# Performance work log

Hardware: AMD Instinct MI355X
Metric: run time of the kernel (lower is better)

Reference implementation:

```python
import jax, jax.numpy as jnp
import numpy as np

K = 7
PAD = K // 2
C = 24          # latent_dim
ITERS = 4


def conv2d(x, w, b):
    # x: (B, Cin, H, W), w: (Cout, Cin, kh, kw) -> (B, Cout, H, W), SAME padding
    y = jax.lax.conv_general_dilated(
        x, w, window_strides=(1, 1), padding='SAME',
        dimension_numbers=('NCHW', 'OIHW', 'NCHW'))
    return y + b[None, :, None, None]


def unfold(x, H, W):
    # F.unfold(x, K, padding=PAD).view(B, C, K*K, H, W)
    # ordering: for each channel, kernel offsets row-major (kh outer, kw inner)
    xp = jnp.pad(x, ((0, 0), (0, 0), (PAD, PAD), (PAD, PAD)))
    patches = jnp.stack(
        [xp[:, :, i:i + H, j:j + W] for i in range(K) for j in range(K)],
        axis=2)  # (B, C, K*K, H, W)
    return patches


def setup_inputs() -> dict:
    key = jax.random.key(0)
    ks = jax.random.split(key, 8)
    B, H, W = 2, 256, 256
    depth = jax.random.normal(ks[0], (B, 1, H, W), dtype=jnp.float32)
    texture = jax.random.normal(ks[1], (B, 3, H, W), dtype=jnp.float32)
    # depth_proj: Conv2d(1, C, 3, padding=1)
    w_dp = jax.random.normal(ks[2], (C, 1, 3, 3), dtype=jnp.float32) * 0.1
    b_dp = jax.random.normal(ks[3], (C,), dtype=jnp.float32) * 0.1
    # kernel_predictor: Conv2d(3, C*K*K, 3, padding=1) followed by softmax(dim=1)
    w_kp = jax.random.normal(ks[4], (C * K * K, 3, 3, 3), dtype=jnp.float32) * 0.1
    b_kp = jax.random.normal(ks[5], (C * K * K,), dtype=jnp.float32) * 0.1
    # to_depth: Conv2d(C, 1, 1)
    w_td = jax.random.normal(ks[6], (1, C, 1, 1), dtype=jnp.float32) * 0.1
    b_td = jax.random.normal(ks[7], (1,), dtype=jnp.float32) * 0.1
    return {'depth': depth, 'texture': texture,
            'w_dp': w_dp, 'b_dp': b_dp,
            'w_kp': w_kp, 'b_kp': b_kp,
            'w_td': w_td, 'b_td': b_td}


def reference(depth, texture, w_dp, b_dp, w_kp, b_kp, w_td, b_td):
    B, _, H, W = depth.shape
    depth_latent = conv2d(depth, w_dp, b_dp)                    # (B, C, H, W)
    logits = conv2d(texture, w_kp, b_kp)                        # (B, C*K*K, H, W)
    kernels = jax.nn.softmax(logits, axis=1)                    # softmax over full channel dim
    kernels = kernels.reshape(B, C, K * K, H, W)
    unfolded = unfold(depth_latent, H, W)                       # (B, C, K*K, H, W)
    for it in range(ITERS):
        diffused = jnp.sum(kernels * unfolded, axis=2)          # (B, C, H, W)
        if it < ITERS - 1:
            unfolded = unfold(diffused, H, W)
    fused_depth = conv2d(diffused, w_td, b_td)                  # (B, 1, H, W)
    return fused_depth
```

## Files before the change

kernel.cpp:

```cpp
#include <hip/hip_runtime.h>

#define BB   2
#define HH   256
#define WW   256
#define HWSZ (HH * WW)
#define CC   24
#define KSZ  7
#define KK   49
#define PADK 3
#define G    8
#define CPG  3
#define LSTR 24
#define CSTR (22 * LSTR)
#define LOG2E 1.44269504088896340736f

typedef __attribute__((ext_vector_type(8))) short short8;
typedef __attribute__((ext_vector_type(4))) float float4v;

__device__ __forceinline__ short f2bf(float x) {
  unsigned u = __builtin_bit_cast(unsigned, x);
  unsigned r = u + 0x7FFFu + ((u >> 16) & 1u);
  return (short)(r >> 16);
}
__device__ __forceinline__ float bf2f(short h) {
  unsigned u = ((unsigned)(unsigned short)h) << 16;
  return __builtin_bit_cast(float, u);
}

__global__ __launch_bounds__(256) void k_setup(
    const float* __restrict__ w_kp, const float* __restrict__ b_kp,
    const float* __restrict__ tex, short* __restrict__ wsW,
    short* __restrict__ wsB) {
  __shared__ float lt[3 * 324];
  __shared__ int lltk[32];
  int blk = blockIdx.x;
  if (blk < 192) {
    int s = blk & 1, mt = (blk >> 1) & 3, cg = blk >> 3;
    for (int idx = threadIdx.x; idx < 512; idx += 256) {
      int row = idx >> 5, k = idx & 31;
      int kk = mt * 16 + row;
      float v = 0.f;
      if (kk < KK && k < 28)
        v = ((k < 27) ? w_kp[((size_t)cg * KK + kk) * 27 + k]
                      : b_kp[cg * KK + kk]) * LOG2E;
      short hi = f2bf(v);
      short h = (s == 0) ? hi : f2bf(v - bf2f(hi));
      wsW[(size_t)blk * 512 + idx] = h;
    }
    return;
  }
  int tb = blk - 192;
  int b = tb >> 8, tile = tb & 255;
  int y0 = (tile >> 4) * 16, x0 = (tile & 15) * 16;
  int tid = threadIdx.x, lane = tid & 63, wv = tid >> 6;
  int q = lane >> 4, col = lane & 15;

  if (tid < 32) {
    int k = tid, v;
    if (k < 27) v = (k / 9) * 324 + ((k % 9) / 3) * 18 + (k % 3);
    else if (k == 27) v = -1;
    else v = -2;
    lltk[k] = v;
  }
  for (int idx = tid; idx < 972; idx += 256) {
    int ci = idx / 324, r = idx % 324;
    int iy = r / 18, ix = r % 18;
    int yy = y0 + iy - 1, xx = x0 + ix - 1;
    bool ok = (yy >= 0 && yy < HH && xx >= 0 && xx < WW);
    lt[idx] = ok ? tex[((size_t)b * 3 + ci) * HWSZ + yy * WW + xx] : 0.f;
  }
  __syncthreads();

  int tko[8];
#pragma unroll
  for (int j = 0; j < 8; ++j) tko[j] = lltk[q * 8 + j];
  int4* w4 = (int4*)wsB;
#pragma unroll
  for (int nt = 0; nt < 4; ++nt) {
    short8 hi, lo;
#pragma unroll
    for (int j = 0; j < 8; ++j) {
      int o = tko[j];
      float v = (o == -1) ? 1.f
                          : ((o == -2) ? 0.f : lt[o + (wv * 4 + nt) * 18 + col]);
      short h = f2bf(v);
      hi[j] = h;
      lo[j] = f2bf(v - bf2f(h));
    }
    size_t base = ((((size_t)(b * 256 + tile) * 4 + wv) * 4 + nt) * 2);
    w4[(base + 0) * 64 + lane] = __builtin_bit_cast(int4, hi);
    w4[(base + 1) * 64 + lane] = __builtin_bit_cast(int4, lo);
  }
}

template <bool FIRST, bool FINAL>
__global__ __launch_bounds__(256, 4) void k_diffuse_m(
    const float* __restrict__ depth, const float* __restrict__ src,
    const float* __restrict__ invZ, const float* __restrict__ w_dp,
    const float* __restrict__ b_dp, const short* __restrict__ wsW,
    const short* __restrict__ wsB, float* __restrict__ dst,
    float* __restrict__ part, const float* __restrict__ w_td,
    float* __restrict__ outp) {
  __shared__ __align__(16) short lw[24 * 512];
  __shared__ float lsrc[CPG * CSTR];
  __shared__ float ldp[FIRST ? 576 : 4];
  __shared__ int loffs[64];

  int b = blockIdx.z / G, g = blockIdx.z % G, c0 = g * CPG;
  int x0 = blockIdx.x * 16, y0 = blockIdx.y * 16;
  int tile = blockIdx.y * 16 + blockIdx.x;
  int tid = threadIdx.x, lane = tid & 63, wv = tid >> 6;
  int q = lane >> 4, col = lane & 15;

  if (tid < 64)
    loffs[tid] = (tid < KK) ? ((tid / 7) - 3) * LSTR + ((tid % 7) - 3) : 0;
  {
    const int4* s4 = (const int4*)(wsW + (size_t)g * 12288);
    int4* d4 = (int4*)lw;
#pragma unroll
    for (int i = 0; i < 6; ++i) d4[tid + i * 256] = s4[tid + i * 256];
  }
  if (FIRST) {
    for (int idx = tid; idx < 576; idx += 256) {
      int iy = idx / 24, ix = idx % 24;
      int yy = y0 + iy - 4, xx = x0 + ix - 4;
      bool ok = (yy >= 0 && yy < HH && xx >= 0 && xx < WW);
      ldp[idx] = ok ? depth[(size_t)b * HWSZ + yy * WW + xx] : 0.f;
    }
  }
  __syncthreads();

  for (int idx = tid; idx < 484; idx += 256) {
    int iy = idx / 22, ix = idx % 22;
    int yy = y0 + iy - PADK, xx = x0 + ix - PADK;
    bool ok = (yy >= 0 && yy < HH && xx >= 0 && xx < WW);
    if (FIRST) {
#pragma unroll
      for (int c = 0; c < CPG; ++c) {
        float a = b_dp[c0 + c];
#pragma unroll
        for (int dy = 0; dy < 3; ++dy)
#pragma unroll
          for (int dx = 0; dx < 3; ++dx)
            a = fmaf(w_dp[(c0 + c) * 9 + dy * 3 + dx],
                     ldp[(iy + dy) * 24 + (ix + dx)], a);
        lsrc[c * CSTR + iy * LSTR + ix] = ok ? a : 0.f;
      }
    } else {
      float sc = ok ? invZ[b * HWSZ + yy * WW + xx] : 0.f;
#pragma unroll
      for (int c = 0; c < CPG; ++c)
        lsrc[c * CSTR + iy * LSTR + ix] =
            ok ? src[((size_t)b * CC + c0 + c) * HWSZ + yy * WW + xx] * sc : 0.f;
    }
  }
  __syncthreads();

  const int4* wB = (const int4*)wsB + ((size_t)(b * 256 + tile) * 4 + wv) * 512;

#pragma unroll 1
  for (int np = 0; np < 2; ++np) {
    short8 Bh0 = __builtin_bit_cast(short8, wB[(np * 4 + 0) * 64 + lane]);
    short8 Bl0 = __builtin_bit_cast(short8, wB[(np * 4 + 1) * 64 + lane]);
    short8 Bh1 = __builtin_bit_cast(short8, wB[(np * 4 + 2) * 64 + lane]);
    short8 Bl1 = __builtin_bit_cast(short8, wB[(np * 4 + 3) * 64 + lane]);
    int basep = (wv * 4 + np * 2 + 3) * LSTR + col + 3;
    float zacc[2] = {0.f, 0.f}, res[2] = {0.f, 0.f};
    float accc[2] = {0.f, 0.f};

    const short* lAp = lw + col * 32 + q * 8;
#pragma unroll 1
    for (int idx = 0; idx < 12; ++idx) {
      short8 Ah = *(const short8*)(lAp);
      short8 Al = *(const short8*)(lAp + 512);
      lAp += 1024;
      int c = idx >> 2, mt = idx & 3;
      int mtb = mt * 16 + q * 4;
      const float* lsc = lsrc + c * CSTR + basep;
      const float* p0 = lsc + loffs[mtb + 0];
      const float* p1 = lsc + loffs[mtb + 1];
      const float* p2 = lsc + loffs[mtb + 2];
      const float* p3 = lsc + loffs[mtb + 3];

      float4v C0 = {0.f, 0.f, 0.f, 0.f}, C1 = {0.f, 0.f, 0.f, 0.f};
      C0 = __builtin_amdgcn_mfma_f32_16x16x32_bf16(Ah, Bh0, C0, 0, 0, 0);
      C1 = __builtin_amdgcn_mfma_f32_16x16x32_bf16(Ah, Bh1, C1, 0, 0, 0);
      C0 = __builtin_amdgcn_mfma_f32_16x16x32_bf16(Ah, Bl0, C0, 0, 0, 0);
      C1 = __builtin_amdgcn_mfma_f32_16x16x32_bf16(Ah, Bl1, C1, 0, 0, 0);
      C0 = __builtin_amdgcn_mfma_f32_16x16x32_bf16(Al, Bh0, C0, 0, 0, 0);
      C1 = __builtin_amdgcn_mfma_f32_16x16x32_bf16(Al, Bh1, C1, 0, 0, 0);

      if (mt < 3) {
        float e00 = __builtin_amdgcn_exp2f(C0[0]);
        float e01 = __builtin_amdgcn_exp2f(C0[1]);
        float e02 = __builtin_amdgcn_exp2f(C0[2]);
        float e03 = __builtin_amdgcn_exp2f(C0[3]);
        float e10 = __builtin_amdgcn_exp2f(C1[0]);
        float e11 = __builtin_amdgcn_exp2f(C1[1]);
        float e12 = __builtin_amdgcn_exp2f(C1[2]);
        float e13 = __builtin_amdgcn_exp2f(C1[3]);
        if (FIRST) {
          zacc[0] += (e00 + e01) + (e02 + e03);
          zacc[1] += (e10 + e11) + (e12 + e13);
        }
        float a0 = accc[0], a1 = accc[1];
        a0 = fmaf(e00, p0[0], a0); a1 = fmaf(e10, p0[LSTR], a1);
        a0 = fmaf(e01, p1[0], a0); a1 = fmaf(e11, p1[LSTR], a1);
        a0 = fmaf(e02, p2[0], a0); a1 = fmaf(e12, p2[LSTR], a1);
        a0 = fmaf(e03, p3[0], a0); a1 = fmaf(e13, p3[LSTR], a1);
        accc[0] = a0; accc[1] = a1;
      } else {
        float e0 = (q == 0) ? __builtin_amdgcn_exp2f(C0[0]) : 0.f;
        float e1 = (q == 0) ? __builtin_amdgcn_exp2f(C1[0]) : 0.f;
        if (FIRST) { zacc[0] += e0; zacc[1] += e1; }
        accc[0] = fmaf(e0, p0[0], accc[0]);
        accc[1] = fmaf(e1, p0[LSTR], accc[1]);
      }
      if (mt == 3) {
#pragma unroll
        for (int t = 0; t < 2; ++t) {
          float v = accc[t];
          v += __shfl_xor(v, 16, 64);
          v += __shfl_xor(v, 32, 64);
          if (FINAL) {
            res[t] = fmaf(w_td[c0 + c], v, res[t]);
          } else {
            int p = (y0 + wv * 4 + np * 2 + t) * WW + (x0 + col);
            if (lane < 16) dst[((size_t)b * CC + c0 + c) * HWSZ + p] = v;
          }
          accc[t] = 0.f;
        }
      }
    }
#pragma unroll
    for (int t = 0; t < 2; ++t) {
      int p = (y0 + wv * 4 + np * 2 + t) * WW + (x0 + col);
      if (FIRST) {
        float z = zacc[t];
        z += __shfl_xor(z, 16, 64);
        z += __shfl_xor(z, 32, 64);
        if (lane < 16) part[(size_t)g * BB * HWSZ + b * HWSZ + p] = z;
      }
      if (FINAL) {
        if (lane < 16) {
          float iz = invZ[b * HWSZ + p];
          atomicAdd(&outp[(size_t)b * HWSZ + p], res[t] * iz);
        }
      }
    }
  }
}

__global__ __launch_bounds__(256) void k_zred(const float* __restrict__ zpart,
                                              float* __restrict__ invZ,
                                              const float* __restrict__ b_td,
                                              float* __restrict__ outp) {
  int t = blockIdx.x * 256 + threadIdx.x;
  float z = 0.f;
#pragma unroll
  for (int g = 0; g < G; ++g) z += zpart[(size_t)g * BB * HWSZ + t];
  invZ[t] = 1.f / z;
  outp[t] = b_td[0];
}

extern "C" void kernel_launch(void* const* d_in, const int* in_sizes, int n_in,
                              void* d_out, int out_size, void* d_ws, size_t ws_size,
                              hipStream_t stream) {
  const float* depth = (const float*)d_in[0];
  const float* tex   = (const float*)d_in[1];
  const float* w_dp  = (const float*)d_in[2];
  const float* b_dp  = (const float*)d_in[3];
  const float* w_kp  = (const float*)d_in[4];
  const float* b_kp  = (const float*)d_in[5];
  const float* w_td  = (const float*)d_in[6];
  const float* b_td  = (const float*)d_in[7];
  float* out = (float*)d_out;

  char* ws = (char*)d_ws;
  const size_t buf_b = (size_t)BB * CC * HWSZ * 4;
  float* bufA = (float*)ws;
  float* bufB = (float*)(ws + buf_b);
  float* part = (float*)(ws + 2 * buf_b);
  float* invZ = (float*)(ws + 2 * buf_b + (size_t)G * BB * HWSZ * 4);
  short* wsW  = (short*)(ws + 2 * buf_b + (size_t)G * BB * HWSZ * 4 +
                         (size_t)BB * HWSZ * 4);
  short* wsB  = (short*)(ws + 2 * buf_b + (size_t)G * BB * HWSZ * 4 +
                         (size_t)BB * HWSZ * 4 + 192 * 512 * 2);

  k_setup<<<dim3(192 + 512), dim3(256), 0, stream>>>(w_kp, b_kp, tex, wsW, wsB);

  dim3 grid(WW / 16, HH / 16, BB * G), blk(256);
  dim3 grid1(BB * HWSZ / 256), blk1(256);

  k_diffuse_m<true, false><<<grid, blk, 0, stream>>>(
      depth, nullptr, nullptr, w_dp, b_dp, wsW, wsB, bufB, part, w_td, nullptr);
  k_zred<<<grid1, blk1, 0, stream>>>(part, invZ, b_td, out);
  k_diffuse_m<false, false><<<grid, blk, 0, stream>>>(
      depth, bufB, invZ, w_dp, b_dp, wsW, wsB, bufA, part, w_td, nullptr);
  k_diffuse_m<false, false><<<grid, blk, 0, stream>>>(
      depth, bufA, invZ, w_dp, b_dp, wsW, wsB, bufB, part, w_td, nullptr);
  k_diffuse_m<false, true><<<grid, blk, 0, stream>>>(
      depth, bufB, invZ, w_dp, b_dp, wsW, wsB, nullptr, part, w_td, out);
}
```

Before: 280.6 us.

## Precompute tap offsets in registers, relayout A weights, unroll inner tap loop

The kernel-predictor weight matrix is stored in a lane-contiguous layout, so each lane reads its 8 bf16 A values with a single contiguous 16-byte LDS load at lane*8. The per-tap LDS offset table is replaced by 16 offsets computed once per thread in registers with a multiply-shift trick. The combined 12-iteration channel/m-tile loop is split into a channel loop with a fully unrolled m-tile loop. Together these drop the offset-table LDS reads and index arithmetic and give the scheduler more MFMA/exp overlap, at the cost of extra register pressure under the 4-blocks-per-CU launch bound.

```diff
diff --git a/kernel.cpp b/kernel.cpp
--- a/kernel.cpp
+++ b/kernel.cpp
@@ -37,8 +37,9 @@
   if (blk < 192) {
     int s = blk & 1, mt = (blk >> 1) & 3, cg = blk >> 3;
     for (int idx = threadIdx.x; idx < 512; idx += 256) {
-      int row = idx >> 5, k = idx & 31;
-      int kk = mt * 16 + row;
+      int l = idx >> 3, j = idx & 7;
+      int kk = mt * 16 + (l & 15);
+      int k = (l >> 4) * 8 + j;
       float v = 0.f;
       if (kk < KK && k < 28)
         v = ((k < 27) ? w_kp[((size_t)cg * KK + kk) * 27 + k]
@@ -104,7 +105,6 @@
   __shared__ __align__(16) short lw[24 * 512];
   __shared__ float lsrc[CPG * CSTR];
   __shared__ float ldp[FIRST ? 576 : 4];
-  __shared__ int loffs[64];
 
   int b = blockIdx.z / G, g = blockIdx.z % G, c0 = g * CPG;
   int x0 = blockIdx.x * 16, y0 = blockIdx.y * 16;
@@ -112,8 +112,6 @@
   int tid = threadIdx.x, lane = tid & 63, wv = tid >> 6;
   int q = lane >> 4, col = lane & 15;
 
-  if (tid < 64)
-    loffs[tid] = (tid < KK) ? ((tid / 7) - 3) * LSTR + ((tid % 7) - 3) : 0;
   {
     const int4* s4 = (const int4*)(wsW + (size_t)g * 12288);
     int4* d4 = (int4*)lw;
@@ -156,6 +154,16 @@
   }
   __syncthreads();
 
+  int offs[16];
+#pragma unroll
+  for (int j = 0; j < 16; ++j) {
+    int t = (j >> 2) * 16 + q * 4 + (j & 3);
+    t = (t < 48) ? t : 48;
+    int dy = (t * 37) >> 8;
+    offs[j] = t + 17 * dy - 75;
+  }
+
+  const short* lA = lw + lane * 8;
   const int4* wB = (const int4*)wsB + ((size_t)(b * 256 + tile) * 4 + wv) * 512;
 
 #pragma unroll 1
@@ -164,73 +172,72 @@
     short8 Bl0 = __builtin_bit_cast(short8, wB[(np * 4 + 1) * 64 + lane]);
     short8 Bh1 = __builtin_bit_cast(short8, wB[(np * 4 + 2) * 64 + lane]);
     short8 Bl1 = __builtin_bit_cast(short8, wB[(np * 4 + 3) * 64 + lane]);
-    int basep = (wv * 4 + np * 2 + 3) * LSTR + col + 3;
+    const float* base = lsrc + (wv * 4 + np * 2 + 3) * LSTR + col + 3;
     float zacc[2] = {0.f, 0.f}, res[2] = {0.f, 0.f};
     float accc[2] = {0.f, 0.f};
 
-    const short* lAp = lw + col * 32 + q * 8;
 #pragma unroll 1
-    for (int idx = 0; idx < 12; ++idx) {
-      short8 Ah = *(const short8*)(lAp);
-      short8 Al = *(const short8*)(lAp + 512);
-      lAp += 1024;
-      int c = idx >> 2, mt = idx & 3;
-      int mtb = mt * 16 + q * 4;
-      const float* lsc = lsrc + c * CSTR + basep;
-      const float* p0 = lsc + loffs[mtb + 0];
-      const float* p1 = lsc + loffs[mtb + 1];
-      const float* p2 = lsc + loffs[mtb + 2];
-      const float* p3 = lsc + loffs[mtb + 3];
-
-      float4v C0 = {0.f, 0.f, 0.f, 0.f}, C1 = {0.f, 0.f, 0.f, 0.f};
-      C0 = __builtin_amdgcn_mfma_f32_16x16x32_bf16(Ah, Bh0, C0, 0, 0, 0);
-      C1 = __builtin_amdgcn_mfma_f32_16x16x32_bf16(Ah, Bh1, C1, 0, 0, 0);
-      C0 = __builtin_amdgcn_mfma_f32_16x16x32_bf16(Ah, Bl0, C0, 0, 0, 0);
-      C1 = __builtin_amdgcn_mfma_f32_16x16x32_bf16(Ah, Bl1, C1, 0, 0, 0);
-      C0 = __builtin_amdgcn_mfma_f32_16x16x32_bf16(Al, Bh0, C0, 0, 0, 0);
-      C1 = __builtin_amdgcn_mfma_f32_16x16x32_bf16(Al, Bh1, C1, 0, 0, 0);
-
-      if (mt < 3) {
-        float e00 = __builtin_amdgcn_exp2f(C0[0]);
-        float e01 = __builtin_amdgcn_exp2f(C0[1]);
-        float e02 = __builtin_amdgcn_exp2f(C0[2]);
-        float e03 = __builtin_amdgcn_exp2f(C0[3]);
-        float e10 = __builtin_amdgcn_exp2f(C1[0]);
-        float e11 = __builtin_amdgcn_exp2f(C1[1]);
-        float e12 = __builtin_amdgcn_exp2f(C1[2]);
-        float e13 = __builtin_amdgcn_exp2f(C1[3]);
-        if (FIRST) {
-          zacc[0] += (e00 + e01) + (e02 + e03);
-          zacc[1] += (e10 + e11) + (e12 + e13);
+    for (int c = 0; c < CPG; ++c) {
+      const short* lAc = lA + c * 2048;
+#pragma unroll
+      for (int mt = 0; mt < 4; ++mt) {
+        short8 Ah = *(const short8*)(lAc + mt * 1024);
+        short8 Al = *(const short8*)(lAc + mt * 1024 + 512);
+
+        float4v C0 = {0.f, 0.f, 0.f, 0.f}, C1 = {0.f, 0.f, 0.f, 0.f};
+        C0 = __builtin_amdgcn_mfma_f32_16x16x32_bf16(Ah, Bh0, C0, 0, 0, 0);
+        C1 = __builtin_amdgcn_mfma_f32_16x16x32_bf16(Ah, Bh1, C1, 0, 0, 0);
+        C0 = __builtin_amdgcn_mfma_f32_16x16x32_bf16(Ah, Bl0, C0, 0, 0, 0);
+        C1 = __builtin_amdgcn_mfma_f32_16x16x32_bf16(Ah, Bl1, C1, 0, 0, 0);
+        C0 = __builtin_amdgcn_mfma_f32_16x16x32_bf16(Al, Bh0, C0, 0, 0, 0);
+        C1 = __builtin_amdgcn_mfma_f32_16x16x32_bf16(Al, Bh1, C1, 0, 0, 0);
+
+        if (mt < 3) {
+          const float* t0 = base + offs[mt * 4 + 0];
+          const float* t1 = base + offs[mt * 4 + 1];
+          const float* t2 = base + offs[mt * 4 + 2];
+          const float* t3 = base + offs[mt * 4 + 3];
+          float e00 = __builtin_amdgcn_exp2f(C0[0]);
+          float e01 = __builtin_amdgcn_exp2f(C0[1]);
+          float e02 = __builtin_amdgcn_exp2f(C0[2]);
+          float e03 = __builtin_amdgcn_exp2f(C0[3]);
+          float e10 = __builtin_amdgcn_exp2f(C1[0]);
+          float e11 = __builtin_amdgcn_exp2f(C1[1]);
+          float e12 = __builtin_amdgcn_exp2f(C1[2]);
+          float e13 = __builtin_amdgcn_exp2f(C1[3]);
+          if (FIRST) {
+            zacc[0] += (e00 + e01) + (e02 + e03);
+            zacc[1] += (e10 + e11) + (e12 + e13);
+          }
+          float a0 = accc[0], a1 = accc[1];
+          a0 = fmaf(e00, t0[0], a0); a1 = fmaf(e10, t0[LSTR], a1);
+          a0 = fmaf(e01, t1[0], a0); a1 = fmaf(e11, t1[LSTR], a1);
+          a0 = fmaf(e02, t2[0], a0); a1 = fmaf(e12, t2[LSTR], a1);
+          a0 = fmaf(e03, t3[0], a0); a1 = fmaf(e13, t3[LSTR], a1);
+          accc[0] = a0; accc[1] = a1;
+        } else {
+          const float* t0 = base + offs[12];
+          float e0 = (q == 0) ? __builtin_amdgcn_exp2f(C0[0]) : 0.f;
+          float e1 = (q == 0) ? __builtin_amdgcn_exp2f(C1[0]) : 0.f;
+          if (FIRST) { zacc[0] += e0; zacc[1] += e1; }
+          accc[0] = fmaf(e0, t0[0], accc[0]);
+          accc[1] = fmaf(e1, t0[LSTR], accc[1]);
         }
-        float a0 = accc[0], a1 = accc[1];
-        a0 = fmaf(e00, p0[0], a0); a1 = fmaf(e10, p0[LSTR], a1);
-        a0 = fmaf(e01, p1[0], a0); a1 = fmaf(e11, p1[LSTR], a1);
-        a0 = fmaf(e02, p2[0], a0); a1 = fmaf(e12, p2[LSTR], a1);
-        a0 = fmaf(e03, p3[0], a0); a1 = fmaf(e13, p3[LSTR], a1);
-        accc[0] = a0; accc[1] = a1;
-      } else {
-        float e0 = (q == 0) ? __builtin_amdgcn_exp2f(C0[0]) : 0.f;
-        float e1 = (q == 0) ? __builtin_amdgcn_exp2f(C1[0]) : 0.f;
-        if (FIRST) { zacc[0] += e0; zacc[1] += e1; }
-        accc[0] = fmaf(e0, p0[0], accc[0]);
-        accc[1] = fmaf(e1, p0[LSTR], accc[1]);
-      }
-      if (mt == 3) {
-#pragma unroll
-        for (int t = 0; t < 2; ++t) {
-          float v = accc[t];
-          v += __shfl_xor(v, 16, 64);
-          v += __shfl_xor(v, 32, 64);
-          if (FINAL) {
-            res[t] = fmaf(w_td[c0 + c], v, res[t]);
-          } else {
-            int p = (y0 + wv * 4 + np * 2 + t) * WW + (x0 + col);
-            if (lane < 16) dst[((size_t)b * CC + c0 + c) * HWSZ + p] = v;
-          }
-          accc[t] = 0.f;
+      }
+#pragma unroll
+      for (int t = 0; t < 2; ++t) {
+        float v = accc[t];
+        v += __shfl_xor(v, 16, 64);
+        v += __shfl_xor(v, 32, 64);
+        if (FINAL) {
+          res[t] = fmaf(w_td[c0 + c], v, res[t]);
+        } else {
+          int p = (y0 + wv * 4 + np * 2 + t) * WW + (x0 + col);
+          if (lane < 16) dst[((size_t)b * CC + c0 + c) * HWSZ + p] = v;
         }
-      }
+        accc[t] = 0.f;
+      }
+      base += CSTR;
     }
 #pragma unroll
     for (int t = 0; t < 2; ++t) {
```

After: 255.6 us. -8.9%, faster.
